# Performance work log

Measured on AMD Instinct MI355X. Metric: run time of the kernel, lower is better.

## Reference

```python
import jax, jax.numpy as jnp
import numpy as np

B, T, I, H, O = 65536, 9, 57, 2, 1


def setup_inputs() -> dict:
    key = jax.random.key(0)
    ks = jax.random.split(key, 8)
    s_ih = 1.0 / np.sqrt(H)  # torch default init scale for GRU/Linear
    x = jax.random.normal(ks[0], (B, T, I), dtype=jnp.float32)
    W_ih = jax.random.uniform(ks[1], (3 * H, I), jnp.float32, -s_ih, s_ih)
    W_hh = jax.random.uniform(ks[2], (3 * H, H), jnp.float32, -s_ih, s_ih)
    b_ih = jax.random.uniform(ks[3], (3 * H,), jnp.float32, -s_ih, s_ih)
    b_hh = jax.random.uniform(ks[4], (3 * H,), jnp.float32, -s_ih, s_ih)
    fc_w = jax.random.uniform(ks[5], (O, H), jnp.float32, -s_ih, s_ih)
    fc_b = jax.random.uniform(ks[6], (O,), jnp.float32, -s_ih, s_ih)
    return {"x": x, "W_ih": W_ih, "W_hh": W_hh, "b_ih": b_ih,
            "b_hh": b_hh, "fc_w": fc_w, "fc_b": fc_b}


def _gru_last_hidden(x, W_ih, W_hh, b_ih, b_hh):
    # Precompute input-side gate projections for all timesteps: [B, T, 3H]
    gx = jnp.einsum('bti,gi->btg', x, W_ih) + b_ih

    def step(h, gxt):
        gh = h @ W_hh.T + b_hh                      # [B, 3H]
        r = jax.nn.sigmoid(gxt[:, :H] + gh[:, :H])
        z = jax.nn.sigmoid(gxt[:, H:2 * H] + gh[:, H:2 * H])
        n = jnp.tanh(gxt[:, 2 * H:] + r * gh[:, 2 * H:])
        h_new = (1.0 - z) * n + z * h
        return h_new, None

    h0 = jnp.zeros((x.shape[0], H), dtype=x.dtype)
    hT, _ = jax.lax.scan(step, h0, jnp.swapaxes(gx, 0, 1))  # scan over time
    return hT                                                # [B, H]


def reference(x, W_ih, W_hh, b_ih, b_hh, fc_w, fc_b):
    hT = _gru_last_hidden(x, W_ih, W_hh, b_ih, b_hh)
    return hT @ fc_w.T + fc_b  # [B, O], fc applied only to last timestep
```

## Files before the change

kernel.cpp:

```cpp
#include <hip/hip_runtime.h>
#include <math.h>


#define T_STEPS 9
#define I_DIM   57
#define ROW_F   513
#define TILE_F  (64 * I_DIM)

__device__ __forceinline__ float sigm(float x) {
    return 1.0f / (1.0f + __expf(-x));
}
__device__ __forceinline__ float tanh_fast(float x) {
    x = fminf(fmaxf(x, -15.0f), 15.0f);
    float e = __expf(2.0f * x);
    return (e - 1.0f) / (e + 1.0f);
}

__global__ __launch_bounds__(64, 2) void gru_kernel(
    const float* __restrict__ x,
    const float* __restrict__ Wih,
    const float* __restrict__ Whh,
    const float* __restrict__ bih,
    const float* __restrict__ bhh,
    const float* __restrict__ fcw,
    const float* __restrict__ fcb,
    float* __restrict__ out)
{
    __shared__ float tile[2][TILE_F];
    const int lane = threadIdx.x;
    const int blk  = blockIdx.x;
    const char* xblk = (const char*)(x + (size_t)blk * 64 * ROW_F);

    int offB[I_DIM];
    {
        int row = (lane >= I_DIM) ? 1 : 0;
        int col = lane - row * I_DIM;
#pragma unroll
        for (int k = 0; k < I_DIM; ++k) {
            offB[k] = row * (ROW_F * 4) + col * 4;
            int c2 = col + 7;
            if (c2 >= I_DIM) { row += 2; col = c2 - I_DIM; }
            else             { row += 1; col = c2; }
        }
    }

    auto issue_tile = [&](int t, int buf) {
        const char* base = xblk + t * (I_DIM * 4);
#pragma unroll
        for (int k = 0; k < I_DIM; ++k) {
            __builtin_amdgcn_global_load_lds(
                (const __attribute__((address_space(1))) void*)(base + offB[k]),
                (__attribute__((address_space(3))) void*)(&tile[buf][64 * k]),
                4, 0, 0);
        }
    };

    issue_tile(0, 0);

    const float b0 = bih[0], b1 = bih[1], b2 = bih[2],
                b3 = bih[3], b4 = bih[4], b5 = bih[5];
    const float c0 = bhh[0], c1 = bhh[1], c2 = bhh[2],
                c3 = bhh[3], c4 = bhh[4], c5 = bhh[5];
    const float w00 = Whh[0],  w01 = Whh[1];
    const float w10 = Whh[2],  w11 = Whh[3];
    const float w20 = Whh[4],  w21 = Whh[5];
    const float w30 = Whh[6],  w31 = Whh[7];
    const float w40 = Whh[8],  w41 = Whh[9];
    const float w50 = Whh[10], w51 = Whh[11];

    float h0 = 0.0f, h1 = 0.0f;

#pragma unroll 1
    for (int t = 0; t < T_STEPS; ++t) {
        __syncthreads();
        if (t + 1 < T_STEPS) issue_tile(t + 1, (t + 1) & 1);

        const float* rowp = &tile[t & 1][lane * I_DIM];
        float xr[I_DIM];
#pragma unroll
        for (int i = 0; i < I_DIM; ++i) xr[i] = rowp[i];

        float a0 = b0, a1 = b1, a2 = b2, a3 = b3, a4 = b4, a5 = b5;
        {
            const float* wg = Wih + 0 * I_DIM;
#pragma unroll
            for (int i = 0; i < I_DIM; ++i) a0 = fmaf(xr[i], wg[i], a0);
        }
        {
            const float* wg = Wih + 1 * I_DIM;
#pragma unroll
            for (int i = 0; i < I_DIM; ++i) a1 = fmaf(xr[i], wg[i], a1);
        }
        {
            const float* wg = Wih + 2 * I_DIM;
#pragma unroll
            for (int i = 0; i < I_DIM; ++i) a2 = fmaf(xr[i], wg[i], a2);
        }
        {
            const float* wg = Wih + 3 * I_DIM;
#pragma unroll
            for (int i = 0; i < I_DIM; ++i) a3 = fmaf(xr[i], wg[i], a3);
        }
        {
            const float* wg = Wih + 4 * I_DIM;
#pragma unroll
            for (int i = 0; i < I_DIM; ++i) a4 = fmaf(xr[i], wg[i], a4);
        }
        {
            const float* wg = Wih + 5 * I_DIM;
#pragma unroll
            for (int i = 0; i < I_DIM; ++i) a5 = fmaf(xr[i], wg[i], a5);
        }

        const float g0 = c0 + w00 * h0 + w01 * h1;
        const float g1 = c1 + w10 * h0 + w11 * h1;
        const float g2 = c2 + w20 * h0 + w21 * h1;
        const float g3 = c3 + w30 * h0 + w31 * h1;
        const float g4 = c4 + w40 * h0 + w41 * h1;
        const float g5 = c5 + w50 * h0 + w51 * h1;

        const float r0 = sigm(a0 + g0);
        const float r1 = sigm(a1 + g1);
        const float z0 = sigm(a2 + g2);
        const float z1 = sigm(a3 + g3);
        const float n0 = tanh_fast(a4 + r0 * g4);
        const float n1 = tanh_fast(a5 + r1 * g5);
        h0 = (1.0f - z0) * n0 + z0 * h0;
        h1 = (1.0f - z1) * n1 + z1 * h1;
    }

    out[blk * 64 + lane] = fcw[0] * h0 + fcw[1] * h1 + fcb[0];
}

extern "C" void kernel_launch(void* const* d_in, const int* in_sizes, int n_in,
                              void* d_out, int out_size, void* d_ws, size_t ws_size,
                              hipStream_t stream) {
    const float* x   = (const float*)d_in[0];
    const float* Wih = (const float*)d_in[1];
    const float* Whh = (const float*)d_in[2];
    const float* bih = (const float*)d_in[3];
    const float* bhh = (const float*)d_in[4];
    const float* fcw = (const float*)d_in[5];
    const float* fcb = (const float*)d_in[6];
    float* out = (float*)d_out;

    gru_kernel<<<dim3(1024), dim3(64), 0, stream>>>(
        x, Wih, Whh, bih, bhh, fcw, fcb, out);
}
```

Baseline: 212.2 us.

## Split GRU hidden units across two wavefronts exchanging state via shared memory

Each block now runs two wavefronts, one per hidden unit. Each wavefront computes three of the six input-gate dot products and its own gate math, and the two exchange hidden values through a double-buffered LDS array each timestep. The tile loads are split between the wavefronts, and each dot product uses two accumulators to shorten the FMA dependency chain. The point is to halve per-thread compute and add latency hiding. In exchange, both waves read the same x row from LDS (doubling LDS traffic), and the per-step barrier now also synchronises the cross-wave hidden-state exchange.

```diff
diff --git a/kernel.cpp b/kernel.cpp
--- a/kernel.cpp
+++ b/kernel.cpp
@@ -6,6 +6,7 @@
 #define I_DIM   57
 #define ROW_F   513
 #define TILE_F  (64 * I_DIM)
+#define NK      29
 
 __device__ __forceinline__ float sigm(float x) {
     return 1.0f / (1.0f + __expf(-x));
@@ -16,7 +17,7 @@
     return (e - 1.0f) / (e + 1.0f);
 }
 
-__global__ __launch_bounds__(64, 2) void gru_kernel(
+__global__ __launch_bounds__(128, 2) void gru_kernel(
     const float* __restrict__ x,
     const float* __restrict__ Wih,
     const float* __restrict__ Whh,
@@ -27,52 +28,56 @@
     float* __restrict__ out)
 {
     __shared__ float tile[2][TILE_F];
-    const int lane = threadIdx.x;
+    __shared__ float hx[2][2][64];
+    const int lane = threadIdx.x & 63;
+    const int w    = __builtin_amdgcn_readfirstlane(threadIdx.x >> 6);
     const int blk  = blockIdx.x;
     const char* xblk = (const char*)(x + (size_t)blk * 64 * ROW_F);
 
-    int offB[I_DIM];
+    int offB[NK];
     {
-        int row = (lane >= I_DIM) ? 1 : 0;
-        int col = lane - row * I_DIM;
+        const int f0 = w * 64 + lane;
+        int row = (f0 >= 2 * I_DIM) ? 2 : ((f0 >= I_DIM) ? 1 : 0);
+        int col = f0 - row * I_DIM;
 #pragma unroll
-        for (int k = 0; k < I_DIM; ++k) {
+        for (int k = 0; k < NK; ++k) {
             offB[k] = row * (ROW_F * 4) + col * 4;
-            int c2 = col + 7;
-            if (c2 >= I_DIM) { row += 2; col = c2 - I_DIM; }
-            else             { row += 1; col = c2; }
+            row += 2; col += 14;
+            if (col >= I_DIM) { row += 1; col -= I_DIM; }
         }
     }
 
     auto issue_tile = [&](int t, int buf) {
         const char* base = xblk + t * (I_DIM * 4);
 #pragma unroll
-        for (int k = 0; k < I_DIM; ++k) {
-            __builtin_amdgcn_global_load_lds(
-                (const __attribute__((address_space(1))) void*)(base + offB[k]),
-                (__attribute__((address_space(3))) void*)(&tile[buf][64 * k]),
-                4, 0, 0);
+        for (int k = 0; k < NK; ++k) {
+            if (2 * k + w < I_DIM) {
+                __builtin_amdgcn_global_load_lds(
+                    (const __attribute__((address_space(1))) void*)(base + offB[k]),
+                    (__attribute__((address_space(3))) void*)(&tile[buf][64 * (2 * k + w)]),
+                    4, 0, 0);
+            }
         }
     };
 
     issue_tile(0, 0);
+    hx[0][w][lane] = 0.0f;
 
-    const float b0 = bih[0], b1 = bih[1], b2 = bih[2],
-                b3 = bih[3], b4 = bih[4], b5 = bih[5];
-    const float c0 = bhh[0], c1 = bhh[1], c2 = bhh[2],
-                c3 = bhh[3], c4 = bhh[4], c5 = bhh[5];
-    const float w00 = Whh[0],  w01 = Whh[1];
-    const float w10 = Whh[2],  w11 = Whh[3];
-    const float w20 = Whh[4],  w21 = Whh[5];
-    const float w30 = Whh[6],  w31 = Whh[7];
-    const float w40 = Whh[8],  w41 = Whh[9];
-    const float w50 = Whh[10], w51 = Whh[11];
+    const float* WR = Wih + (0 + w) * I_DIM;
+    const float* WZ = Wih + (2 + w) * I_DIM;
+    const float* WN = Wih + (4 + w) * I_DIM;
+    const float bR = bih[0 + w], bZ = bih[2 + w], bN = bih[4 + w];
+    const float cR = bhh[0 + w], cZ = bhh[2 + w], cN = bhh[4 + w];
+    const float wr0 = Whh[(0 + w) * 2], wr1 = Whh[(0 + w) * 2 + 1];
+    const float wz0 = Whh[(2 + w) * 2], wz1 = Whh[(2 + w) * 2 + 1];
+    const float wn0 = Whh[(4 + w) * 2], wn1 = Whh[(4 + w) * 2 + 1];
 
-    float h0 = 0.0f, h1 = 0.0f;
+    float hm = 0.0f;
 
 #pragma unroll 1
     for (int t = 0; t < T_STEPS; ++t) {
         __syncthreads();
+        const float ho = hx[t & 1][1 - w][lane];
         if (t + 1 < T_STEPS) issue_tile(t + 1, (t + 1) & 1);
 
         const float* rowp = &tile[t & 1][lane * I_DIM];
@@ -80,56 +85,52 @@
 #pragma unroll
         for (int i = 0; i < I_DIM; ++i) xr[i] = rowp[i];
 
-        float a0 = b0, a1 = b1, a2 = b2, a3 = b3, a4 = b4, a5 = b5;
-        {
-            const float* wg = Wih + 0 * I_DIM;
+        float r0 = bR, r1 = 0.0f;
 #pragma unroll
-            for (int i = 0; i < I_DIM; ++i) a0 = fmaf(xr[i], wg[i], a0);
+        for (int i = 0; i < I_DIM - 1; i += 2) {
+            r0 = fmaf(xr[i],     WR[i],     r0);
+            r1 = fmaf(xr[i + 1], WR[i + 1], r1);
         }
-        {
-            const float* wg = Wih + 1 * I_DIM;
+        r0 = fmaf(xr[I_DIM - 1], WR[I_DIM - 1], r0);
+        const float aR = r0 + r1;
+
+        float z0 = bZ, z1 = 0.0f;
 #pragma unroll
-            for (int i = 0; i < I_DIM; ++i) a1 = fmaf(xr[i], wg[i], a1);
+        for (int i = 0; i < I_DIM - 1; i += 2) {
+            z0 = fmaf(xr[i],     WZ[i],     z0);
+            z1 = fmaf(xr[i + 1], WZ[i + 1], z1);
         }
-        {
-            const float* wg = Wih + 2 * I_DIM;
+        z0 = fmaf(xr[I_DIM - 1], WZ[I_DIM - 1], z0);
+        const float aZ = z0 + z1;
+
+        float n0 = bN, n1 = 0.0f;
 #pragma unroll
-            for (int i = 0; i < I_DIM; ++i) a2 = fmaf(xr[i], wg[i], a2);
+        for (int i = 0; i < I_DIM - 1; i += 2) {
+            n0 = fmaf(xr[i],     WN[i],     n0);
+            n1 = fmaf(xr[i + 1], WN[i + 1], n1);
         }
-        {
-            const float* wg = Wih + 3 * I_DIM;
-#pragma unroll
-            for (int i = 0; i < I_DIM; ++i) a3 = fmaf(xr[i], wg[i], a3);
-        }
-        {
-            const float* wg = Wih + 4 * I_DIM;
-#pragma unroll
-            for (int i = 0; i < I_DIM; ++i) a4 = fmaf(xr[i], wg[i], a4);
-        }
-        {
-            const float* wg = Wih + 5 * I_DIM;
-#pragma unroll
-            for (int i = 0; i < I_DIM; ++i) a5 = fmaf(xr[i], wg[i], a5);
-        }
+        n0 = fmaf(xr[I_DIM - 1], WN[I_DIM - 1], n0);
+        const float aN = n0 + n1;
 
-        const float g0 = c0 + w00 * h0 + w01 * h1;
-        const float g1 = c1 + w10 * h0 + w11 * h1;
-        const float g2 = c2 + w20 * h0 + w21 * h1;
-        const float g3 = c3 + w30 * h0 + w31 * h1;
-        const float g4 = c4 + w40 * h0 + w41 * h1;
-        const float g5 = c5 + w50 * h0 + w51 * h1;
+        const float h0 = w ? ho : hm;
+        const float h1 = w ? hm : ho;
+        const float gR = cR + wr0 * h0 + wr1 * h1;
+        const float gZ = cZ + wz0 * h0 + wz1 * h1;
+        const float gN = cN + wn0 * h0 + wn1 * h1;
 
-        const float r0 = sigm(a0 + g0);
-        const float r1 = sigm(a1 + g1);
-        const float z0 = sigm(a2 + g2);
-        const float z1 = sigm(a3 + g3);
-        const float n0 = tanh_fast(a4 + r0 * g4);
-        const float n1 = tanh_fast(a5 + r1 * g5);
-        h0 = (1.0f - z0) * n0 + z0 * h0;
-        h1 = (1.0f - z1) * n1 + z1 * h1;
+        const float r = sigm(aR + gR);
+        const float z = sigm(aZ + gZ);
+        const float n = tanh_fast(aN + r * gN);
+        hm = (1.0f - z) * n + z * hm;
+
+        hx[(t + 1) & 1][w][lane] = hm;
     }
 
-    out[blk * 64 + lane] = fcw[0] * h0 + fcw[1] * h1 + fcb[0];
+    __syncthreads();
+    if (w == 0) {
+        const float h1f = hx[T_STEPS & 1][1][lane];
+        out[blk * 64 + lane] = fcw[0] * hm + fcw[1] * h1f + fcb[0];
+    }
 }
 
 extern "C" void kernel_launch(void* const* d_in, const int* in_sizes, int n_in,
@@ -144,6 +145,6 @@
     const float* fcb = (const float*)d_in[6];
     float* out = (float*)d_out;
 
-    gru_kernel<<<dim3(1024), dim3(64), 0, stream>>>(
+    gru_kernel<<<dim3(1024), dim3(128), 0, stream>>>(
         x, Wih, Whh, bih, bhh, fcw, fcb, out);
 }
```

Measured after the change: 211.4 us. Within noise of the previous version (-0.4%).

## Replace LDS staging with per-thread register double-buffered direct global loads

Applied to the files above, without the earlier changes.

Drops the shared-memory tile and the global_load_lds async copy. Each thread now loads its own row's timestep slice straight into registers, using two register arrays as a ping-pong buffer so the next timestep's load overlaps the current step's compute. The block barrier goes away, launch bounds drop to one block per CU to allow more registers, and each dot product is split into two accumulators to shorten the FMA dependency chain. The trade-off is uncoalesced strided per-thread global loads (lanes are 513 floats apart) and higher register pressure in exchange for no LDS traffic and no synchronization.

```diff
diff --git a/kernel.cpp b/kernel.cpp
--- a/kernel.cpp
+++ b/kernel.cpp
@@ -5,7 +5,6 @@
 #define T_STEPS 9
 #define I_DIM   57
 #define ROW_F   513
-#define TILE_F  (64 * I_DIM)
 
 __device__ __forceinline__ float sigm(float x) {
     return 1.0f / (1.0f + __expf(-x));
@@ -16,7 +15,7 @@
     return (e - 1.0f) / (e + 1.0f);
 }
 
-__global__ __launch_bounds__(64, 2) void gru_kernel(
+__global__ __launch_bounds__(64, 1) void gru_kernel(
     const float* __restrict__ x,
     const float* __restrict__ Wih,
     const float* __restrict__ Whh,
@@ -26,36 +25,9 @@
     const float* __restrict__ fcb,
     float* __restrict__ out)
 {
-    __shared__ float tile[2][TILE_F];
     const int lane = threadIdx.x;
-    const int blk  = blockIdx.x;
-    const char* xblk = (const char*)(x + (size_t)blk * 64 * ROW_F);
-
-    int offB[I_DIM];
-    {
-        int row = (lane >= I_DIM) ? 1 : 0;
-        int col = lane - row * I_DIM;
-#pragma unroll
-        for (int k = 0; k < I_DIM; ++k) {
-            offB[k] = row * (ROW_F * 4) + col * 4;
-            int c2 = col + 7;
-            if (c2 >= I_DIM) { row += 2; col = c2 - I_DIM; }
-            else             { row += 1; col = c2; }
-        }
-    }
-
-    auto issue_tile = [&](int t, int buf) {
-        const char* base = xblk + t * (I_DIM * 4);
-#pragma unroll
-        for (int k = 0; k < I_DIM; ++k) {
-            __builtin_amdgcn_global_load_lds(
-                (const __attribute__((address_space(1))) void*)(base + offB[k]),
-                (__attribute__((address_space(3))) void*)(&tile[buf][64 * k]),
-                4, 0, 0);
-        }
-    };
-
-    issue_tile(0, 0);
+    const int b    = blockIdx.x * 64 + lane;
+    const float* __restrict__ row = x + (size_t)b * ROW_F;
 
     const float b0 = bih[0], b1 = bih[1], b2 = bih[2],
                 b3 = bih[3], b4 = bih[4], b5 = bih[5];
@@ -69,67 +41,105 @@
     const float w50 = Whh[10], w51 = Whh[11];
 
     float h0 = 0.0f, h1 = 0.0f;
+    float xa[I_DIM], xb[I_DIM];
 
-#pragma unroll 1
-    for (int t = 0; t < T_STEPS; ++t) {
-        __syncthreads();
-        if (t + 1 < T_STEPS) issue_tile(t + 1, (t + 1) & 1);
+    auto load_ts = [&](float (&d)[I_DIM], const float* p) {
+#pragma unroll
+        for (int i = 0; i < I_DIM; ++i) d[i] = p[i];
+    };
 
-        const float* rowp = &tile[t & 1][lane * I_DIM];
-        float xr[I_DIM];
-#pragma unroll
-        for (int i = 0; i < I_DIM; ++i) xr[i] = rowp[i];
-
-        float a0 = b0, a1 = b1, a2 = b2, a3 = b3, a4 = b4, a5 = b5;
+    auto step = [&](const float (&xr)[I_DIM]) {
+        float aR0 = b0, aR1 = 0.0f;
         {
             const float* wg = Wih + 0 * I_DIM;
 #pragma unroll
-            for (int i = 0; i < I_DIM; ++i) a0 = fmaf(xr[i], wg[i], a0);
+            for (int i = 0; i < I_DIM - 1; i += 2) {
+                aR0 = fmaf(xr[i],     wg[i],     aR0);
+                aR1 = fmaf(xr[i + 1], wg[i + 1], aR1);
+            }
+            aR0 = fmaf(xr[I_DIM - 1], wg[I_DIM - 1], aR0);
         }
+        float aS0 = b1, aS1 = 0.0f;
         {
             const float* wg = Wih + 1 * I_DIM;
 #pragma unroll
-            for (int i = 0; i < I_DIM; ++i) a1 = fmaf(xr[i], wg[i], a1);
+            for (int i = 0; i < I_DIM - 1; i += 2) {
+                aS0 = fmaf(xr[i],     wg[i],     aS0);
+                aS1 = fmaf(xr[i + 1], wg[i + 1], aS1);
+            }
+            aS0 = fmaf(xr[I_DIM - 1], wg[I_DIM - 1], aS0);
         }
+        float aZ0 = b2, aZ1 = 0.0f;
         {
             const float* wg = Wih + 2 * I_DIM;
 #pragma unroll
-            for (int i = 0; i < I_DIM; ++i) a2 = fmaf(xr[i], wg[i], a2);
+            for (int i = 0; i < I_DIM - 1; i += 2) {
+                aZ0 = fmaf(xr[i],     wg[i],     aZ0);
+                aZ1 = fmaf(xr[i + 1], wg[i + 1], aZ1);
+            }
+            aZ0 = fmaf(xr[I_DIM - 1], wg[I_DIM - 1], aZ0);
         }
+        float aY0 = b3, aY1 = 0.0f;
         {
             const float* wg = Wih + 3 * I_DIM;
 #pragma unroll
-            for (int i = 0; i < I_DIM; ++i) a3 = fmaf(xr[i], wg[i], a3);
+            for (int i = 0; i < I_DIM - 1; i += 2) {
+                aY0 = fmaf(xr[i],     wg[i],     aY0);
+                aY1 = fmaf(xr[i + 1], wg[i + 1], aY1);
+            }
+            aY0 = fmaf(xr[I_DIM - 1], wg[I_DIM - 1], aY0);
         }
+        float aN0 = b4, aN1 = 0.0f;
         {
             const float* wg = Wih + 4 * I_DIM;
 #pragma unroll
-            for (int i = 0; i < I_DIM; ++i) a4 = fmaf(xr[i], wg[i], a4);
+            for (int i = 0; i < I_DIM - 1; i += 2) {
+                aN0 = fmaf(xr[i],     wg[i],     aN0);
+                aN1 = fmaf(xr[i + 1], wg[i + 1], aN1);
+            }
+            aN0 = fmaf(xr[I_DIM - 1], wg[I_DIM - 1], aN0);
         }
+        float aM0 = b5, aM1 = 0.0f;
         {
             const float* wg = Wih + 5 * I_DIM;
 #pragma unroll
-            for (int i = 0; i < I_DIM; ++i) a5 = fmaf(xr[i], wg[i], a5);
+            for (int i = 0; i < I_DIM - 1; i += 2) {
+                aM0 = fmaf(xr[i],     wg[i],     aM0);
+                aM1 = fmaf(xr[i + 1], wg[i + 1], aM1);
+            }
+            aM0 = fmaf(xr[I_DIM - 1], wg[I_DIM - 1], aM0);
         }
 
-        const float g0 = c0 + w00 * h0 + w01 * h1;
-        const float g1 = c1 + w10 * h0 + w11 * h1;
-        const float g2 = c2 + w20 * h0 + w21 * h1;
-        const float g3 = c3 + w30 * h0 + w31 * h1;
-        const float g4 = c4 + w40 * h0 + w41 * h1;
-        const float g5 = c5 + w50 * h0 + w51 * h1;
+        const float gR = c0 + w00 * h0 + w01 * h1;
+        const float gS = c1 + w10 * h0 + w11 * h1;
+        const float gZ = c2 + w20 * h0 + w21 * h1;
+        const float gY = c3 + w30 * h0 + w31 * h1;
+        const float gN = c4 + w40 * h0 + w41 * h1;
+        const float gM = c5 + w50 * h0 + w51 * h1;
 
-        const float r0 = sigm(a0 + g0);
-        const float r1 = sigm(a1 + g1);
-        const float z0 = sigm(a2 + g2);
-        const float z1 = sigm(a3 + g3);
-        const float n0 = tanh_fast(a4 + r0 * g4);
-        const float n1 = tanh_fast(a5 + r1 * g5);
+        const float r0 = sigm((aR0 + aR1) + gR);
+        const float r1 = sigm((aS0 + aS1) + gS);
+        const float z0 = sigm((aZ0 + aZ1) + gZ);
+        const float z1 = sigm((aY0 + aY1) + gY);
+        const float n0 = tanh_fast((aN0 + aN1) + r0 * gN);
+        const float n1 = tanh_fast((aM0 + aM1) + r1 * gM);
         h0 = (1.0f - z0) * n0 + z0 * h0;
         h1 = (1.0f - z1) * n1 + z1 * h1;
+    };
+
+    load_ts(xa, row);
+    const float* p = row;
+#pragma unroll 1
+    for (int t = 0; t < T_STEPS - 1; t += 2) {
+        load_ts(xb, p + I_DIM);
+        step(xa);
+        load_ts(xa, p + 2 * I_DIM);
+        step(xb);
+        p += 2 * I_DIM;
     }
+    step(xa);
 
-    out[blk * 64 + lane] = fcw[0] * h0 + fcw[1] * h1 + fcb[0];
+    out[b] = fcw[0] * h0 + fcw[1] * h1 + fcb[0];
 }
 
 extern "C" void kernel_launch(void* const* d_in, const int* in_sizes, int n_in,
```

After: 211.7 us. About the same (-0.2%).
